# Optimization experiments

Hardware: AMD Instinct MI355X
Metric: run time of the kernel (lower is better)

Reference implementation:

```python
import jax, jax.numpy as jnp
import numpy as np
import math

STRIDES = [8, 16, 32, 64, 128]
NUM_CLASSES = 80
NUM_ANCHORS = 9
_RATIOS = np.array([0.5, 1.0, 2.0])
_SCALES = 2.0 ** np.array([0.0, 1.0 / 3.0, 2.0 / 3.0])


def _base_anchors(base_size):
    # standard RetinaNet base anchors: 3 ratios x 3 scales, centered at origin
    a = np.zeros((9, 4))
    a[:, 2:] = base_size * np.tile(_SCALES, (2, 3)).T
    areas = a[:, 2] * a[:, 3]
    a[:, 2] = np.sqrt(areas / np.repeat(_RATIOS, 3))
    a[:, 3] = a[:, 2] * np.repeat(_RATIOS, 3)
    a[:, 0::2] -= np.tile(a[:, 2] * 0.5, (2, 1)).T
    a[:, 1::2] -= np.tile(a[:, 3] * 0.5, (2, 1)).T
    return a


def _make_anchors(featmap_sizes):
    per_level = []
    for (h, w), s in zip(featmap_sizes, STRIDES):
        base = _base_anchors(4 * s)  # base_size = 4 * stride (RetinaNet convention)
        sx = (np.arange(w) + 0.5) * s
        sy = (np.arange(h) + 0.5) * s
        X, Y = np.meshgrid(sx, sy)
        shifts = np.stack([X.ravel(), Y.ravel(), X.ravel(), Y.ravel()], axis=1)
        # anchors vary fastest per location -> matches [B,H,W,A,*] flatten order
        per_level.append((shifts[:, None, :] + base[None, :, :]).reshape(-1, 4))
    return jnp.asarray(np.concatenate(per_level, axis=0), dtype=jnp.float32)


def _conv3x3(x, w, b):
    y = jax.lax.conv_general_dilated(x, w, (1, 1), 'SAME', dimension_numbers=('NCHW', 'OIHW', 'NCHW'))
    return y + b[None, :, None, None]


def _tower(x, ws, bs):
    for i in range(4):
        x = jax.nn.relu(_conv3x3(x, ws[i], bs[i]))
    return _conv3x3(x, ws[4], bs[4])


def _bbox_transform(anchors, deltas):
    # BBoxTransform with mean 0, std (0.1, 0.1, 0.2, 0.2)
    w = anchors[:, 2] - anchors[:, 0]
    h = anchors[:, 3] - anchors[:, 1]
    cx = anchors[:, 0] + 0.5 * w
    cy = anchors[:, 1] + 0.5 * h
    pcx = cx + deltas[..., 0] * 0.1 * w
    pcy = cy + deltas[..., 1] * 0.1 * h
    pw = jnp.exp(deltas[..., 2] * 0.2) * w
    ph = jnp.exp(deltas[..., 3] * 0.2) * h
    return jnp.stack([pcx - 0.5 * pw, pcy - 0.5 * ph, pcx + 0.5 * pw, pcy + 0.5 * ph], axis=-1)


def _heads(feats, cls_ws, cls_bs, reg_ws, reg_bs):
    B = feats[0].shape[0]
    cls_l, reg_l = [], []
    for f in feats:
        c = _tower(f, cls_ws, cls_bs)  # [B, 9*80, H, W]
        cls_l.append(jnp.transpose(c, (0, 2, 3, 1)).reshape(B, -1, NUM_CLASSES))
        r = _tower(f, reg_ws, reg_bs)  # [B, 9*4, H, W]
        reg_l.append(jnp.transpose(r, (0, 2, 3, 1)).reshape(B, -1, 4))
    return jnp.concatenate(cls_l, axis=1), jnp.concatenate(reg_l, axis=1)


def setup_inputs():
    key = jax.random.key(0)
    ks = jax.random.split(key, 32)
    B, C = 8, 256
    sizes = [(64, 64), (32, 32), (16, 16), (8, 8), (4, 4)]
    inp = {}
    for i, (h, w) in enumerate(sizes):
        inp['feat%d' % i] = jax.random.normal(ks[i], (B, C, h, w), dtype=jnp.float32)
    prior_bias = -math.log((1.0 - 0.01) / 0.01)

    def mk(k, out_ch, in_ch):
        std = math.sqrt(2.0 / (9.0 * out_ch))  # matches torch init normal_(0, sqrt(2/n))
        return jax.random.normal(k, (out_ch, in_ch, 3, 3), dtype=jnp.float32) * std

    ki = 5
    for i in range(4):
        inp['cls_w%d' % i] = mk(ks[ki], 256, 256); ki += 1
        inp['cls_b%d' % i] = jnp.zeros((256,), jnp.float32)
    inp['cls_w4'] = mk(ks[ki], NUM_ANCHORS * NUM_CLASSES, 256); ki += 1
    inp['cls_b4'] = jnp.full((NUM_ANCHORS * NUM_CLASSES,), prior_bias, jnp.float32)
    for i in range(4):
        inp['reg_w%d' % i] = mk(ks[ki], 256, 256); ki += 1
        inp['reg_b%d' % i] = jnp.zeros((256,), jnp.float32)
    inp['reg_w4'] = mk(ks[ki], NUM_ANCHORS * 4, 256); ki += 1
    inp['reg_b4'] = jnp.full((NUM_ANCHORS * 4,), prior_bias, jnp.float32)
    return inp


def reference(feat0, feat1, feat2, feat3, feat4,
              cls_w0, cls_b0, cls_w1, cls_b1, cls_w2, cls_b2, cls_w3, cls_b3, cls_w4, cls_b4,
              reg_w0, reg_b0, reg_w1, reg_b1, reg_w2, reg_b2, reg_w3, reg_b3, reg_w4, reg_b4):
    feats = [feat0, feat1, feat2, feat3, feat4]
    cls_ws = [cls_w0, cls_w1, cls_w2, cls_w3, cls_w4]
    cls_bs = [cls_b0, cls_b1, cls_b2, cls_b3, cls_b4]
    reg_ws = [reg_w0, reg_w1, reg_w2, reg_w3, reg_w4]
    reg_bs = [reg_b0, reg_b1, reg_b2, reg_b3, reg_b4]
    pred_cls, pred_reg = _heads(feats, cls_ws, cls_bs, reg_ws, reg_bs)
    anchors = _make_anchors([f.shape[-2:] for f in feats])  # [A, 4]
    boxes = _bbox_transform(anchors, pred_reg)  # [B, A, 4]
    probs = jax.nn.sigmoid(pred_cls)  # [B, A, 80]
    scores = jnp.max(probs, axis=2)
    class_id = jnp.argmax(probs, axis=2)
    return scores, class_id, boxes
```

## Files before the change

kernel.cpp:

```cpp
#include <hip/hip_runtime.h>
#include <math.h>

#define CIN 256
#define TLW 16
#define TLH 8
#define LIS 20

template<typename TI, typename TA, int CH, bool RELU>
__global__ __launch_bounds__(256) void conv_tile(
    const TI* __restrict__ in, const float* __restrict__ wgt,
    const float* __restrict__ bias, TA* __restrict__ out,
    int H, int W, int C_out)
{
    const int NCH = CIN / CH;
    const int tilesX = (W + TLW - 1) / TLW;
    const int tx = (blockIdx.x % tilesX) * TLW;
    const int ty = (blockIdx.x / tilesX) * TLH;
    const int b  = blockIdx.y;
    const int co0 = blockIdx.z * 64;
    const int tid = threadIdx.x;
    const int tco = (tid >> 5) * 8;
    const int tpx = tid & 31;
    const int prow = tpx >> 2;
    const int pcol = (tpx & 3) * 4;

    __shared__ __align__(16) TA lw[CH * 9 * 64];
    __shared__ __align__(16) TA li[CH * 10 * LIS];

    TA acc[8][4];
    #pragma unroll
    for (int c = 0; c < 8; ++c)
        #pragma unroll
        for (int j = 0; j < 4; ++j) acc[c][j] = (TA)0;

    const int coLim = min(64, C_out - co0);

    for (int ch = 0; ch < NCH; ++ch) {
        const int ci0 = ch * CH;
        for (int idx = tid; idx < CH * 9 * 64; idx += 256) {
            int r  = idx >> 6;
            int co = idx & 63;
            TA v = (TA)0;
            if (co < coLim)
                v = (TA)wgt[(size_t)(co0 + co) * (CIN * 9) + (size_t)ci0 * 9 + r];
            lw[idx] = v;
        }
        for (int idx = tid; idx < CH * 10 * LIS; idx += 256) {
            int ci = idx / (10 * LIS);
            int rr = idx % (10 * LIS);
            int row = rr / LIS, col = rr % LIS;
            TA v = (TA)0;
            int iy = ty + row - 1, ix = tx + col - 1;
            if (col < TLW + 2 && iy >= 0 && iy < H && ix >= 0 && ix < W)
                v = (TA)in[(((size_t)b * CIN + ci0 + ci) * H + iy) * W + ix];
            li[idx] = v;
        }
        __syncthreads();
        #pragma unroll
        for (int ci = 0; ci < CH; ++ci) {
            #pragma unroll
            for (int ky = 0; ky < 3; ++ky) {
                const TA* ip = &li[ci * 10 * LIS + (prow + ky) * LIS + pcol];
                TA ir[6];
                #pragma unroll
                for (int t = 0; t < 6; ++t) ir[t] = ip[t];
                #pragma unroll
                for (int kx = 0; kx < 3; ++kx) {
                    const TA* wp = &lw[(ci * 9 + ky * 3 + kx) * 64 + tco];
                    TA wv[8];
                    #pragma unroll
                    for (int c = 0; c < 8; ++c) wv[c] = wp[c];
                    TA x0 = ir[kx], x1 = ir[kx + 1], x2 = ir[kx + 2], x3 = ir[kx + 3];
                    #pragma unroll
                    for (int c = 0; c < 8; ++c) {
                        acc[c][0] += wv[c] * x0;
                        acc[c][1] += wv[c] * x1;
                        acc[c][2] += wv[c] * x2;
                        acc[c][3] += wv[c] * x3;
                    }
                }
            }
        }
        __syncthreads();
    }

    const int oy = ty + prow;
    if (oy < H) {
        #pragma unroll
        for (int c = 0; c < 8; ++c) {
            int co = co0 + tco + c;
            if (co < C_out) {
                TA bv = (TA)bias[co];
                #pragma unroll
                for (int j = 0; j < 4; ++j) {
                    int ox = tx + pcol + j;
                    if (ox < W) {
                        TA v = acc[c][j] + bv;
                        if (RELU) v = v > (TA)0 ? v : (TA)0;
                        out[(((size_t)b * C_out + co) * H + oy) * W + ox] = v;
                    }
                }
            }
        }
    }
}

#define CH5 8
__global__ __launch_bounds__(320) void conv_cls5(
    const double* __restrict__ in, const float* __restrict__ wgt,
    const float* __restrict__ bias, float* __restrict__ scores,
    float* __restrict__ cls_id,
    int H, int W, int level_off, int A_total, int b0)
{
    const int tilesX = (W + TLW - 1) / TLW;
    const int tx = (blockIdx.x % tilesX) * TLW;
    const int ty = (blockIdx.x / tilesX) * TLH;
    const int b  = blockIdx.y;
    const int a  = blockIdx.z;
    const int co0 = a * 80;
    const int tid = threadIdx.x;
    const int tc  = tid >> 4;
    const int tco4 = tc * 4;
    const int tp  = tid & 15;
    const int prow = tp >> 1;
    const int pcol = (tp & 1) * 8;

    __shared__ __align__(16) double lw[CH5 * 9 * 80];
    __shared__ __align__(16) double li[CH5 * 10 * LIS];

    double acc[4][8];
    #pragma unroll
    for (int c = 0; c < 4; ++c)
        #pragma unroll
        for (int j = 0; j < 8; ++j) acc[c][j] = 0.0;

    for (int ch = 0; ch < CIN / CH5; ++ch) {
        const int ci0 = ch * CH5;
        for (int idx = tid; idx < CH5 * 9 * 80; idx += 320) {
            int r  = idx / 80;
            int co = idx % 80;
            lw[idx] = (double)wgt[(size_t)(co0 + co) * (CIN * 9)
                                  + (size_t)ci0 * 9 + r];
        }
        for (int idx = tid; idx < CH5 * 10 * LIS; idx += 320) {
            int ci = idx / (10 * LIS);
            int rr = idx % (10 * LIS);
            int row = rr / LIS, col = rr % LIS;
            double v = 0.0;
            int iy = ty + row - 1, ix = tx + col - 1;
            if (col < TLW + 2 && iy >= 0 && iy < H && ix >= 0 && ix < W)
                v = in[(((size_t)b * CIN + ci0 + ci) * H + iy) * W + ix];
            li[idx] = v;
        }
        __syncthreads();
        #pragma unroll
        for (int ci = 0; ci < CH5; ++ci) {
            #pragma unroll
            for (int ky = 0; ky < 3; ++ky) {
                const double* ip = &li[ci * 10 * LIS + (prow + ky) * LIS + pcol];
                double ir[10];
                #pragma unroll
                for (int t = 0; t < 10; ++t) ir[t] = ip[t];
                #pragma unroll
                for (int kx = 0; kx < 3; ++kx) {
                    const double* wp = &lw[(ci * 9 + ky * 3 + kx) * 80 + tco4];
                    double w0 = wp[0], w1 = wp[1], w2 = wp[2], w3 = wp[3];
                    #pragma unroll
                    for (int j = 0; j < 8; ++j) {
                        double x = ir[kx + j];
                        acc[0][j] += w0 * x;
                        acc[1][j] += w1 * x;
                        acc[2][j] += w2 * x;
                        acc[3][j] += w3 * x;
                    }
                }
            }
        }
        __syncthreads();
    }

    double* redM = lw;
    int*    redA = (int*)li;

    double bv[4];
    #pragma unroll
    for (int c = 0; c < 4; ++c) bv[c] = (double)bias[co0 + tco4 + c];
    #pragma unroll
    for (int j = 0; j < 8; ++j) {
        double m = acc[0][j] + bv[0];
        int am = tco4;
        #pragma unroll
        for (int c = 1; c < 4; ++c) {
            double v = acc[c][j] + bv[c];
            if (v > m) { m = v; am = tco4 + c; }
        }
        int p = prow * 16 + pcol + j;
        redM[p * 20 + tc] = m;
        redA[p * 20 + tc] = am;
    }
    __syncthreads();
    if (tid < 128) {
        int p = tid;
        double m = redM[p * 20]; int am = redA[p * 20];
        #pragma unroll
        for (int t = 1; t < 20; ++t)
            if (redM[p * 20 + t] > m) { m = redM[p * 20 + t]; am = redA[p * 20 + t]; }
        int oy = ty + (p >> 4), ox = tx + (p & 15);
        if (oy < H && ox < W) {
            size_t oi = (size_t)(b0 + b) * A_total + level_off
                      + (size_t)(oy * W + ox) * 9 + a;
            scores[oi] = (float)(1.0 / (1.0 + exp(-m)));
            cls_id[oi] = (float)am;
        }
    }
}

__global__ void boxes_ep(const float* __restrict__ reg5, float* __restrict__ boxes,
                         int H, int W, int level_off, int A_total, float stride,
                         int b0, int Bc)
{
    int idx = blockIdx.x * 256 + threadIdx.x;
    int total = Bc * H * W * 9;
    if (idx >= total) return;
    int a = idx % 9; int rest = idx / 9;
    int x = rest % W; rest /= W;
    int y = rest % H; int b = rest / H;

    float base = 4.f * stride;
    float scale = exp2f((float)(a % 3) * (1.f / 3.f));
    int ri = a / 3;
    float sr = (ri == 0) ? 0.70710678118654752f : (ri == 1 ? 1.f : 1.41421356237309505f);
    float wa = base * scale / sr;
    float ha = base * scale * sr;
    float cx = (x + 0.5f) * stride, cy = (y + 0.5f) * stride;

    size_t cs = (size_t)H * W;
    const float* rp = reg5 + (((size_t)b * 36 + a * 4) * H + y) * W + x;
    float d0 = rp[0], d1 = rp[cs], d2 = rp[2 * cs], d3 = rp[3 * cs];

    float pcx = cx + d0 * 0.1f * wa;
    float pcy = cy + d1 * 0.1f * ha;
    float pw  = expf(d2 * 0.2f) * wa;
    float ph  = expf(d3 * 0.2f) * ha;

    size_t oi = ((size_t)(b0 + b) * A_total + level_off
               + (size_t)(y * W + x) * 9 + a) * 4;
    boxes[oi + 0] = pcx - 0.5f * pw;
    boxes[oi + 1] = pcy - 0.5f * ph;
    boxes[oi + 2] = pcx + 0.5f * pw;
    boxes[oi + 3] = pcy + 0.5f * ph;
}

extern "C" void kernel_launch(void* const* d_in, const int* in_sizes, int n_in,
                              void* d_out, int out_size, void* d_ws, size_t ws_size,
                              hipStream_t stream)
{
    const float* feats[5];
    for (int i = 0; i < 5; ++i) feats[i] = (const float*)d_in[i];
    const float* cw[5]; const float* cb[5];
    const float* rw[5]; const float* rb[5];
    for (int i = 0; i < 5; ++i) {
        cw[i] = (const float*)d_in[5 + 2 * i];
        cb[i] = (const float*)d_in[6 + 2 * i];
        rw[i] = (const float*)d_in[15 + 2 * i];
        rb[i] = (const float*)d_in[16 + 2 * i];
    }

    const int A_total = 49104;
    float* scores = (float*)d_out;
    float* cls_id = scores + (size_t)8 * A_total;
    float* boxes  = scores + (size_t)2 * 8 * A_total;

    const int   Hs[5]      = {64, 32, 16, 8, 4};
    const float strides[5] = {8.f, 16.f, 32.f, 64.f, 128.f};
    const int   offs[5]    = {0, 36864, 46080, 48384, 48960};

    for (int l = 0; l < 5; ++l) {
        int H = Hs[l], W = Hs[l];
        size_t perb = (size_t)CIN * H * W;
        int Bc = 8;
        while (Bc > 1 && 2ull * Bc * perb * sizeof(double) > ws_size) Bc >>= 1;
        double* D0 = (double*)d_ws;
        double* D1 = D0 + (size_t)Bc * perb;
        int tiles = ((W + TLW - 1) / TLW) * ((H + TLH - 1) / TLH);
        for (int b0 = 0; b0 < 8; b0 += Bc) {
            dim3 g(tiles, Bc, 4);
            const float* fin = feats[l] + (size_t)b0 * perb;
            conv_tile<float,  double, 8, true><<<g, 256, 0, stream>>>(fin, cw[0], cb[0], D0, H, W, 256);
            conv_tile<double, double, 8, true><<<g, 256, 0, stream>>>(D0,  cw[1], cb[1], D1, H, W, 256);
            conv_tile<double, double, 8, true><<<g, 256, 0, stream>>>(D1,  cw[2], cb[2], D0, H, W, 256);
            conv_tile<double, double, 8, true><<<g, 256, 0, stream>>>(D0,  cw[3], cb[3], D1, H, W, 256);
            dim3 g5(tiles, Bc, 9);
            conv_cls5<<<g5, 320, 0, stream>>>(D1, cw[4], cb[4], scores, cls_id,
                                              H, W, offs[l], A_total, b0);
        }
    }

    for (int l = 0; l < 5; ++l) {
        int H = Hs[l], W = Hs[l];
        size_t perb = (size_t)CIN * H * W;
        int Br = 8;
        while (Br > 1 && 2ull * Br * perb * sizeof(float) > ws_size) Br >>= 1;
        float* F0 = (float*)d_ws;
        float* F1 = F0 + (size_t)Br * perb;
        int tiles = ((W + TLW - 1) / TLW) * ((H + TLH - 1) / TLH);
        for (int b0 = 0; b0 < 8; b0 += Br) {
            dim3 g(tiles, Br, 4);
            const float* fin = feats[l] + (size_t)b0 * perb;
            conv_tile<float, float, 8, true><<<g, 256, 0, stream>>>(fin, rw[0], rb[0], F0, H, W, 256);
            conv_tile<float, float, 8, true><<<g, 256, 0, stream>>>(F0,  rw[1], rb[1], F1, H, W, 256);
            conv_tile<float, float, 8, true><<<g, 256, 0, stream>>>(F1,  rw[2], rb[2], F0, H, W, 256);
            conv_tile<float, float, 8, true><<<g, 256, 0, stream>>>(F0,  rw[3], rb[3], F1, H, W, 256);
            dim3 gr(tiles, Br, 1);
            conv_tile<float, float, 8, false><<<gr, 256, 0, stream>>>(F1, rw[4], rb[4], F0, H, W, 36);
            int total = Br * H * W * 9;
            boxes_ep<<<(total + 255) / 256, 256, 0, stream>>>(F0, boxes, H, W,
                                                              offs[l], A_total,
                                                              strides[l], b0, Br);
        }
    }
}
```

Baseline: 27.29 ms.

## Remap cls5 conv to 256 threads with 10x4 register tiles, pad LDS rows

Changes the final class conv from 320 threads with 4 channels x 8 pixels per thread to 256 threads with 10 channels x 4 pixels, so the reduction runs over 8 partials per pixel instead of 20. It also adds a min-blocks-per-CU hint of 2 to both conv kernels and widens the shared-memory input row stride from 20 to 22 doubles, aiming to cut bank conflicts. The larger per-thread double accumulator set raises register pressure, and the occupancy hint could force spilling.

```diff
diff --git a/kernel.cpp b/kernel.cpp
--- a/kernel.cpp
+++ b/kernel.cpp
@@ -4,10 +4,10 @@
 #define CIN 256
 #define TLW 16
 #define TLH 8
-#define LIS 20
+#define LIS 22
 
 template<typename TI, typename TA, int CH, bool RELU>
-__global__ __launch_bounds__(256) void conv_tile(
+__global__ __launch_bounds__(256, 2) void conv_tile(
     const TI* __restrict__ in, const float* __restrict__ wgt,
     const float* __restrict__ bias, TA* __restrict__ out,
     int H, int W, int C_out)
@@ -106,7 +106,7 @@
 }
 
 #define CH5 8
-__global__ __launch_bounds__(320) void conv_cls5(
+__global__ __launch_bounds__(256, 2) void conv_cls5(
     const double* __restrict__ in, const float* __restrict__ wgt,
     const float* __restrict__ bias, float* __restrict__ scores,
     float* __restrict__ cls_id,
@@ -119,30 +119,30 @@
     const int a  = blockIdx.z;
     const int co0 = a * 80;
     const int tid = threadIdx.x;
-    const int tc  = tid >> 4;
-    const int tco4 = tc * 4;
-    const int tp  = tid & 15;
-    const int prow = tp >> 1;
-    const int pcol = (tp & 1) * 8;
+    const int cog = tid >> 5;
+    const int tco = cog * 10;
+    const int tpx = tid & 31;
+    const int prow = tpx >> 2;
+    const int pcol = (tpx & 3) * 4;
 
     __shared__ __align__(16) double lw[CH5 * 9 * 80];
     __shared__ __align__(16) double li[CH5 * 10 * LIS];
 
-    double acc[4][8];
+    double acc[10][4];
     #pragma unroll
-    for (int c = 0; c < 4; ++c)
-        #pragma unroll
-        for (int j = 0; j < 8; ++j) acc[c][j] = 0.0;
+    for (int c = 0; c < 10; ++c)
+        #pragma unroll
+        for (int j = 0; j < 4; ++j) acc[c][j] = 0.0;
 
     for (int ch = 0; ch < CIN / CH5; ++ch) {
         const int ci0 = ch * CH5;
-        for (int idx = tid; idx < CH5 * 9 * 80; idx += 320) {
+        for (int idx = tid; idx < CH5 * 9 * 80; idx += 256) {
             int r  = idx / 80;
             int co = idx % 80;
             lw[idx] = (double)wgt[(size_t)(co0 + co) * (CIN * 9)
                                   + (size_t)ci0 * 9 + r];
         }
-        for (int idx = tid; idx < CH5 * 10 * LIS; idx += 320) {
+        for (int idx = tid; idx < CH5 * 10 * LIS; idx += 256) {
             int ci = idx / (10 * LIS);
             int rr = idx % (10 * LIS);
             int row = rr / LIS, col = rr % LIS;
@@ -158,20 +158,22 @@
             #pragma unroll
             for (int ky = 0; ky < 3; ++ky) {
                 const double* ip = &li[ci * 10 * LIS + (prow + ky) * LIS + pcol];
-                double ir[10];
-                #pragma unroll
-                for (int t = 0; t < 10; ++t) ir[t] = ip[t];
+                double ir[6];
+                #pragma unroll
+                for (int t = 0; t < 6; ++t) ir[t] = ip[t];
                 #pragma unroll
                 for (int kx = 0; kx < 3; ++kx) {
-                    const double* wp = &lw[(ci * 9 + ky * 3 + kx) * 80 + tco4];
-                    double w0 = wp[0], w1 = wp[1], w2 = wp[2], w3 = wp[3];
+                    const double* wp = &lw[(ci * 9 + ky * 3 + kx) * 80 + tco];
+                    double wv[10];
                     #pragma unroll
-                    for (int j = 0; j < 8; ++j) {
-                        double x = ir[kx + j];
-                        acc[0][j] += w0 * x;
-                        acc[1][j] += w1 * x;
-                        acc[2][j] += w2 * x;
-                        acc[3][j] += w3 * x;
+                    for (int c = 0; c < 10; ++c) wv[c] = wp[c];
+                    double x0 = ir[kx], x1 = ir[kx + 1], x2 = ir[kx + 2], x3 = ir[kx + 3];
+                    #pragma unroll
+                    for (int c = 0; c < 10; ++c) {
+                        acc[c][0] += wv[c] * x0;
+                        acc[c][1] += wv[c] * x1;
+                        acc[c][2] += wv[c] * x2;
+                        acc[c][3] += wv[c] * x3;
                     }
                 }
             }
@@ -182,29 +184,26 @@
     double* redM = lw;
     int*    redA = (int*)li;
 
-    double bv[4];
     #pragma unroll
-    for (int c = 0; c < 4; ++c) bv[c] = (double)bias[co0 + tco4 + c];
-    #pragma unroll
-    for (int j = 0; j < 8; ++j) {
-        double m = acc[0][j] + bv[0];
-        int am = tco4;
-        #pragma unroll
-        for (int c = 1; c < 4; ++c) {
-            double v = acc[c][j] + bv[c];
-            if (v > m) { m = v; am = tco4 + c; }
+    for (int j = 0; j < 4; ++j) {
+        double m = acc[0][j] + (double)bias[co0 + tco];
+        int am = tco;
+        #pragma unroll
+        for (int c = 1; c < 10; ++c) {
+            double v = acc[c][j] + (double)bias[co0 + tco + c];
+            if (v > m) { m = v; am = tco + c; }
         }
         int p = prow * 16 + pcol + j;
-        redM[p * 20 + tc] = m;
-        redA[p * 20 + tc] = am;
+        redM[p * 8 + cog] = m;
+        redA[p * 8 + cog] = am;
     }
     __syncthreads();
     if (tid < 128) {
         int p = tid;
-        double m = redM[p * 20]; int am = redA[p * 20];
-        #pragma unroll
-        for (int t = 1; t < 20; ++t)
-            if (redM[p * 20 + t] > m) { m = redM[p * 20 + t]; am = redA[p * 20 + t]; }
+        double m = redM[p * 8]; int am = redA[p * 8];
+        #pragma unroll
+        for (int t = 1; t < 8; ++t)
+            if (redM[p * 8 + t] > m) { m = redM[p * 8 + t]; am = redA[p * 8 + t]; }
         int oy = ty + (p >> 4), ox = tx + (p & 15);
         if (oy < H && ox < W) {
             size_t oi = (size_t)(b0 + b) * A_total + level_off
@@ -291,7 +290,7 @@
             conv_tile<double, double, 8, true><<<g, 256, 0, stream>>>(D1,  cw[2], cb[2], D0, H, W, 256);
             conv_tile<double, double, 8, true><<<g, 256, 0, stream>>>(D0,  cw[3], cb[3], D1, H, W, 256);
             dim3 g5(tiles, Bc, 9);
-            conv_cls5<<<g5, 320, 0, stream>>>(D1, cw[4], cb[4], scores, cls_id,
+            conv_cls5<<<g5, 256, 0, stream>>>(D1, cw[4], cb[4], scores, cls_id,
                                               H, W, offs[l], A_total, b0);
         }
     }
```

Measured after the change: 25.01 ms. 1.09x faster.
